# Performance work log

Hardware: AMD Instinct MI355X
Metric: run time of the kernel (lower is better)

## Reference

```python
import jax, jax.numpy as jnp
import numpy as np

LN_EPS = 1e-5

def _layernorm(x, gamma, beta):
    mu = jnp.mean(x, axis=-1, keepdims=True)
    var = jnp.mean((x - mu) ** 2, axis=-1, keepdims=True)
    return (x - mu) * jax.lax.rsqrt(var + LN_EPS) * gamma + beta

def setup_inputs() -> dict:
    key = jax.random.key(0)
    ks = jax.random.split(key, 12)
    n_drug, n_dis, E = 10000, 10000, 1000000
    feat = 128          # in_units * 2
    d_in = 2 * feat     # in_units * 4 = 256
    hid = 128
    hid2 = hid // 2
    def lin(kw, kb, fan_in, fan_out):
        bound = 1.0 / np.sqrt(fan_in)
        W = jax.random.uniform(kw, (fan_in, fan_out), jnp.float32, -bound, bound)
        b = jax.random.uniform(kb, (fan_out,), jnp.float32, -bound, bound)
        return W, b
    W1, b1 = lin(ks[0], ks[1], d_in, hid)
    W2, b2 = lin(ks[2], ks[3], hid, hid2)
    W3, b3 = lin(ks[4], ks[5], hid2, 1)
    return {
        "drug_feat": jax.random.normal(ks[6], (n_drug, feat), jnp.float32),
        "dis_feat": jax.random.normal(ks[7], (n_dis, feat), jnp.float32),
        "src_idx": jax.random.randint(ks[8], (E,), 0, n_drug, jnp.int32),
        "dst_idx": jax.random.randint(ks[9], (E,), 0, n_dis, jnp.int32),
        "W1": W1, "b1": b1,
        "g1": jnp.ones((hid,), jnp.float32), "be1": jnp.zeros((hid,), jnp.float32),
        "W2": W2, "b2": b2,
        "g2": jnp.ones((hid2,), jnp.float32), "be2": jnp.zeros((hid2,), jnp.float32),
        "W3": W3, "b3": b3,
    }

def reference(drug_feat, dis_feat, src_idx, dst_idx,
              W1, b1, g1, be1, W2, b2, g2, be2, W3, b3):
    # apply_edges: gather src (drug) and dst (disease) features, concat -> [E, 4*in_units]
    m = jnp.concatenate([drug_feat[src_idx], dis_feat[dst_idx]], axis=1)
    h = jax.nn.gelu(_layernorm(m @ W1 + b1, g1, be1), approximate=False)
    h = jax.nn.gelu(_layernorm(h @ W2 + b2, g2, be2), approximate=False)
    return h @ W3 + b3  # [E, 1]
```

## Files before the change

### kernel.cpp

```cpp
#include <hip/hip_runtime.h>
#include <hip/hip_bf16.h>

typedef __attribute__((ext_vector_type(4))) float f32x4;
typedef __attribute__((ext_vector_type(8))) short bf16x8;

#define MFMA16(a, b, c) __builtin_amdgcn_mfma_f32_16x16x32_bf16((a), (b), (c), 0, 0, 0)

#define W1T_OFF 0
#define B1_OFF  65536
#define G1_OFF  66048
#define E1_OFF  66560
#define B2_OFF  67072
#define G2_OFF  67328
#define E2_OFF  67584
#define W3_OFF  67840
#define B3_OFF  68096
#define SMEM_BYTES 68128

__device__ __forceinline__ short f2bf(float x) {
  __hip_bfloat16 h = __float2bfloat16(x);
  return __builtin_bit_cast(short, h);
}

__device__ __forceinline__ bf16x8 pack8(f32x4 a, f32x4 b) {
  bf16x8 r;
  r[0] = f2bf(a[0]); r[1] = f2bf(a[1]); r[2] = f2bf(a[2]); r[3] = f2bf(a[3]);
  r[4] = f2bf(b[0]); r[5] = f2bf(b[1]); r[6] = f2bf(b[2]); r[7] = f2bf(b[3]);
  return r;
}

__device__ __forceinline__ float gelu_fast(float z) {
  float s = z * z;
  float y = z * __builtin_fmaf(0.0705657f, s, 1.5976f);
  float t = __expf(-y);
  return z * __builtin_amdgcn_rcpf(1.0f + t);
}

__global__ __launch_bounds__(256) void prep_weights(
    const float* __restrict__ W1, const float* __restrict__ W2,
    short* __restrict__ w1i, short* __restrict__ w2i) {
  int idx = blockIdx.x * 256 + threadIdx.x;
  if (idx < 32768) {
    int k = idx >> 7, n = idx & 127;
    w1i[n * 256 + ((((k >> 3) ^ (n & 7)) << 3) | (k & 7))] = f2bf(W1[idx]);
  } else if (idx < 40960) {
    int j = idx - 32768;
    int n2 = j >> 7, pos = j & 127;
    int kf = ((((pos >> 3) ^ (n2 & 7)) << 3) | (pos & 7));
    int q = (kf >> 3) & 3, kb2 = kf >> 5, e = kf & 7;
    int n = kb2 * 32 + (e >> 2) * 16 + q * 4 + (e & 3);
    w2i[j] = f2bf(W2[n * 64 + n2]);
  }
}

__global__ __launch_bounds__(256) void prep_feats(
    const float* __restrict__ f, short* __restrict__ o, int n8) {
  int idx = blockIdx.x * 256 + threadIdx.x;
  if (idx < n8) {
    f32x4 a = *(const f32x4*)(f + idx * 8);
    f32x4 b = *(const f32x4*)(f + idx * 8 + 4);
    *(bf16x8*)(o + idx * 8) = pack8(a, b);
  }
}

__global__ __launch_bounds__(512, 2) void mlp_fused(
    const short* __restrict__ drugb, const short* __restrict__ disb,
    const int* __restrict__ src, const int* __restrict__ dst,
    const short* __restrict__ w1i, const short* __restrict__ w2i,
    const float* __restrict__ b1, const float* __restrict__ g1, const float* __restrict__ be1,
    const float* __restrict__ b2, const float* __restrict__ g2, const float* __restrict__ be2,
    const float* __restrict__ W3, const float* __restrict__ b3,
    float* __restrict__ out, int E, int ntiles) {
  extern __shared__ char smem[];
  short* w1t = (short*)(smem + W1T_OFF);
  float* b1s = (float*)(smem + B1_OFF);
  float* g1s = (float*)(smem + G1_OFF);
  float* e1s = (float*)(smem + E1_OFF);
  float* b2s = (float*)(smem + B2_OFF);
  float* g2s = (float*)(smem + G2_OFF);
  float* e2s = (float*)(smem + E2_OFF);
  float* w3s = (float*)(smem + W3_OFF);
  float* b3s = (float*)(smem + B3_OFF);

  const int tid  = threadIdx.x;
  const int wave = tid >> 6;
  const int lane = tid & 63;
  const int q    = lane >> 4;
  const int cc   = lane & 15;

  #pragma unroll
  for (int o = 0; o < 8; ++o) {
    int s = (tid + o * 512) * 8;
    *(bf16x8*)(w1t + s) = *(const bf16x8*)(w1i + s);
  }
  if (tid < 128) { b1s[tid] = b1[tid]; g1s[tid] = g1[tid]; e1s[tid] = be1[tid]; }
  else if (tid < 192) { int j = tid - 128; b2s[j] = b2[j]; g2s[j] = g2[j]; e2s[j] = be2[j]; w3s[j] = W3[j]; }
  if (tid == 256) b3s[0] = b3[0];
  __syncthreads();

  const short* w2p = w2i + cc * 128;

  for (int tile = blockIdx.x; tile < ntiles; tile += gridDim.x) {
    const int r  = tile * 128 + wave * 16 + cc;
    const int rc = (r < E) ? r : (E - 1);
    const short* pd = drugb + (size_t)src[rc] * 128 + q * 8;
    const short* pq = disb  + (size_t)dst[rc] * 128 + q * 8;

    f32x4 acc1[8];
    #pragma unroll
    for (int nt = 0; nt < 8; ++nt)
      acc1[nt] = *(const f32x4*)(b1s + nt * 16 + q * 4);

    bf16x8 u = *(const bf16x8*)pd;
    #pragma unroll 1
    for (int kb = 0; kb < 8; ++kb) {
      bf16x8 bfr = u;
      if (kb < 7) {
        const short* pn = (kb < 3) ? (pd + (kb + 1) * 32) : (pq + (kb - 3) * 32);
        u = *(const bf16x8*)pn;
      }
      const char* abase = (const char*)w1t + cc * 512 + ((((kb * 4 + q) ^ (cc & 7))) << 4);
      #pragma unroll
      for (int nt = 0; nt < 8; ++nt) {
        bf16x8 af = *(const bf16x8*)(abase + nt * 8192);
        acc1[nt] = MFMA16(af, bfr, acc1[nt]);
      }
    }

    bf16x8 hreg[4];
    {
      float s = 0.f, ss = 0.f;
      #pragma unroll
      for (int nt = 0; nt < 8; ++nt)
        #pragma unroll
        for (int j = 0; j < 4; ++j) { float v = acc1[nt][j]; s += v; ss += v * v; }
      s  += __shfl_xor(s, 16);  s  += __shfl_xor(s, 32);
      ss += __shfl_xor(ss, 16); ss += __shfl_xor(ss, 32);
      float mu   = s * 0.0078125f;
      float var  = ss * 0.0078125f - mu * mu;
      var = (var > 0.f) ? var : 0.f;
      float rstd = __builtin_amdgcn_rsqf(var + 1e-5f);

      #pragma unroll
      for (int h = 0; h < 4; ++h) {
        f32x4 glo = *(const f32x4*)(g1s + (2 * h) * 16 + q * 4);
        f32x4 elo = *(const f32x4*)(e1s + (2 * h) * 16 + q * 4);
        f32x4 ghi = *(const f32x4*)(g1s + (2 * h + 1) * 16 + q * 4);
        f32x4 ehi = *(const f32x4*)(e1s + (2 * h + 1) * 16 + q * 4);
        f32x4 a, b;
        #pragma unroll
        for (int j = 0; j < 4; ++j) {
          a[j] = gelu_fast(__builtin_fmaf((acc1[2 * h][j] - mu) * rstd, glo[j], elo[j]));
          b[j] = gelu_fast(__builtin_fmaf((acc1[2 * h + 1][j] - mu) * rstd, ghi[j], ehi[j]));
        }
        hreg[h] = pack8(a, b);
      }
    }

    f32x4 acc2[4];
    #pragma unroll
    for (int t = 0; t < 4; ++t)
      acc2[t] = *(const f32x4*)(b2s + t * 16 + q * 4);

    #pragma unroll
    for (int kb2 = 0; kb2 < 4; ++kb2) {
      bf16x8 hb = hreg[kb2];
      const int ch = ((kb2 * 4 + q) ^ (cc & 7));
      #pragma unroll
      for (int t = 0; t < 4; ++t) {
        bf16x8 af = *(const bf16x8*)(w2p + t * 2048 + ch * 8);
        acc2[t] = MFMA16(af, hb, acc2[t]);
      }
      __builtin_amdgcn_sched_barrier(0);
    }

    {
      float s = 0.f, ss = 0.f;
      #pragma unroll
      for (int t = 0; t < 4; ++t)
        #pragma unroll
        for (int j = 0; j < 4; ++j) { float v = acc2[t][j]; s += v; ss += v * v; }
      s  += __shfl_xor(s, 16);  s  += __shfl_xor(s, 32);
      ss += __shfl_xor(ss, 16); ss += __shfl_xor(ss, 32);
      float mu   = s * 0.015625f;
      float var  = ss * 0.015625f - mu * mu;
      var = (var > 0.f) ? var : 0.f;
      float rstd = __builtin_amdgcn_rsqf(var + 1e-5f);

      float dot = 0.f;
      #pragma unroll
      for (int t = 0; t < 4; ++t) {
        f32x4 gv = *(const f32x4*)(g2s + t * 16 + q * 4);
        f32x4 ev = *(const f32x4*)(e2s + t * 16 + q * 4);
        f32x4 wv = *(const f32x4*)(w3s + t * 16 + q * 4);
        #pragma unroll
        for (int j = 0; j < 4; ++j) {
          float zz = __builtin_fmaf((acc2[t][j] - mu) * rstd, gv[j], ev[j]);
          dot = __builtin_fmaf(gelu_fast(zz), wv[j], dot);
        }
      }
      dot += __shfl_xor(dot, 16); dot += __shfl_xor(dot, 32);
      if (q == 0 && r < E) out[r] = dot + b3s[0];
    }
  }
}

extern "C" void kernel_launch(void* const* d_in, const int* in_sizes, int n_in,
                              void* d_out, int out_size, void* d_ws, size_t ws_size,
                              hipStream_t stream) {
  const float* drug = (const float*)d_in[0];
  const float* dis  = (const float*)d_in[1];
  const int*   src  = (const int*)d_in[2];
  const int*   dst  = (const int*)d_in[3];
  const float* W1   = (const float*)d_in[4];
  const float* b1   = (const float*)d_in[5];
  const float* g1   = (const float*)d_in[6];
  const float* be1  = (const float*)d_in[7];
  const float* W2   = (const float*)d_in[8];
  const float* b2   = (const float*)d_in[9];
  const float* g2   = (const float*)d_in[10];
  const float* be2  = (const float*)d_in[11];
  const float* W3   = (const float*)d_in[12];
  const float* b3   = (const float*)d_in[13];
  float* out = (float*)d_out;

  const int E      = in_sizes[2];
  const int ndrug8 = in_sizes[0] / 8;
  const int ndis8  = in_sizes[1] / 8;
  const int ntiles = (E + 127) / 128;

  short* w1i   = (short*)d_ws;
  short* w2i   = w1i + 32768;
  short* drugb = w2i + 8192;
  short* disb  = drugb + (size_t)ndrug8 * 8;

  (void)hipFuncSetAttribute((const void*)mlp_fused,
                            hipFuncAttributeMaxDynamicSharedMemorySize, SMEM_BYTES);

  prep_weights<<<dim3(160), dim3(256), 0, stream>>>(W1, W2, w1i, w2i);
  prep_feats<<<dim3((ndrug8 + 255) / 256), dim3(256), 0, stream>>>(drug, drugb, ndrug8);
  prep_feats<<<dim3((ndis8 + 255) / 256), dim3(256), 0, stream>>>(dis, disb, ndis8);

  int grid = 512;
  if (ntiles < grid) grid = ntiles;
  mlp_fused<<<dim3(grid), dim3(512), SMEM_BYTES, stream>>>(
      drugb, disb, src, dst, w1i, w2i, b1, g1, be1, b2, g2, be2, W3, b3, out, E, ntiles);
}
```

Before: 251.0 us.

## Split W1 between LDS and lane-packed global loads, repack W2 for coalescing

Keeps only the first 192 K-rows of W1 in LDS and pre-packs the last 64 rows and all of W2 in lane-contiguous MFMA fragment order, so each lane reads them from global/L2 with a single coalesced 16-byte load. This shrinks LDS per block (about 68KB to 52KB) and removes the xor-swizzled W2 addressing. GELU now uses exp2 with prescaled constants. The cost is extra global traffic per tile for the W1 tail and W2 fragments, which relies on cache hits.

```diff
diff --git a/kernel.cpp b/kernel.cpp
--- a/kernel.cpp
+++ b/kernel.cpp
@@ -7,15 +7,15 @@
 #define MFMA16(a, b, c) __builtin_amdgcn_mfma_f32_16x16x32_bf16((a), (b), (c), 0, 0, 0)
 
 #define W1T_OFF 0
-#define B1_OFF  65536
-#define G1_OFF  66048
-#define E1_OFF  66560
-#define B2_OFF  67072
-#define G2_OFF  67328
-#define E2_OFF  67584
-#define W3_OFF  67840
-#define B3_OFF  68096
-#define SMEM_BYTES 68128
+#define B1_OFF  49152
+#define G1_OFF  49664
+#define E1_OFF  50176
+#define B2_OFF  50688
+#define G2_OFF  50944
+#define E2_OFF  51200
+#define W3_OFF  51456
+#define B3_OFF  51712
+#define SMEM_BYTES 51744
 
 __device__ __forceinline__ short f2bf(float x) {
   __hip_bfloat16 h = __float2bfloat16(x);
@@ -31,25 +31,37 @@
 
 __device__ __forceinline__ float gelu_fast(float z) {
   float s = z * z;
-  float y = z * __builtin_fmaf(0.0705657f, s, 1.5976f);
-  float t = __expf(-y);
+  float y = z * __builtin_fmaf(-0.10180479f, s, -2.3048496f);
+  float t = __builtin_amdgcn_exp2f(y);
   return z * __builtin_amdgcn_rcpf(1.0f + t);
 }
 
 __global__ __launch_bounds__(256) void prep_weights(
     const float* __restrict__ W1, const float* __restrict__ W2,
-    short* __restrict__ w1i, short* __restrict__ w2i) {
+    short* __restrict__ w1i, short* __restrict__ w1b, short* __restrict__ w2L) {
   int idx = blockIdx.x * 256 + threadIdx.x;
   if (idx < 32768) {
     int k = idx >> 7, n = idx & 127;
-    w1i[n * 256 + ((((k >> 3) ^ (n & 7)) << 3) | (k & 7))] = f2bf(W1[idx]);
+    int chunk = k >> 3, e = k & 7;
+    short v = f2bf(W1[idx]);
+    if (chunk < 24) {
+      int pos = (chunk & 24) | ((chunk & 7) ^ (n & 7));
+      w1i[n * 192 + pos * 8 + e] = v;
+    } else {
+      int kb = chunk >> 2;
+      int qq = chunk & 3;
+      int lane = qq * 16 + (n & 15);
+      int nt = n >> 4;
+      w1b[((kb - 6) * 8 + nt) * 512 + lane * 8 + e] = v;
+    }
   } else if (idx < 40960) {
     int j = idx - 32768;
-    int n2 = j >> 7, pos = j & 127;
-    int kf = ((((pos >> 3) ^ (n2 & 7)) << 3) | (pos & 7));
-    int q = (kf >> 3) & 3, kb2 = kf >> 5, e = kf & 7;
-    int n = kb2 * 32 + (e >> 2) * 16 + q * 4 + (e & 3);
-    w2i[j] = f2bf(W2[n * 64 + n2]);
+    int n = j >> 6, n2 = j & 63;
+    int kb2 = n >> 5;
+    int qf = (n >> 2) & 3;
+    int e = ((n >> 4) & 1) * 4 + (n & 3);
+    int t = n2 >> 4, cc2 = n2 & 15;
+    w2L[(kb2 * 4 + t) * 512 + (qf * 16 + cc2) * 8 + e] = f2bf(W2[j]);
   }
 }
 
@@ -66,7 +78,8 @@
 __global__ __launch_bounds__(512, 2) void mlp_fused(
     const short* __restrict__ drugb, const short* __restrict__ disb,
     const int* __restrict__ src, const int* __restrict__ dst,
-    const short* __restrict__ w1i, const short* __restrict__ w2i,
+    const short* __restrict__ w1i, const short* __restrict__ w1b,
+    const short* __restrict__ w2L,
     const float* __restrict__ b1, const float* __restrict__ g1, const float* __restrict__ be1,
     const float* __restrict__ b2, const float* __restrict__ g2, const float* __restrict__ be2,
     const float* __restrict__ W3, const float* __restrict__ b3,
@@ -89,7 +102,7 @@
   const int cc   = lane & 15;
 
   #pragma unroll
-  for (int o = 0; o < 8; ++o) {
+  for (int o = 0; o < 6; ++o) {
     int s = (tid + o * 512) * 8;
     *(bf16x8*)(w1t + s) = *(const bf16x8*)(w1i + s);
   }
@@ -98,7 +111,8 @@
   if (tid == 256) b3s[0] = b3[0];
   __syncthreads();
 
-  const short* w2p = w2i + cc * 128;
+  const short* w1bp = w1b + (lane << 3);
+  const short* w2p  = w2L + (lane << 3);
 
   for (int tile = blockIdx.x; tile < ntiles; tile += gridDim.x) {
     const int r  = tile * 128 + wave * 16 + cc;
@@ -113,18 +127,30 @@
 
     bf16x8 u = *(const bf16x8*)pd;
     #pragma unroll 1
-    for (int kb = 0; kb < 8; ++kb) {
+    for (int kb = 0; kb < 6; ++kb) {
       bf16x8 bfr = u;
-      if (kb < 7) {
+      {
         const short* pn = (kb < 3) ? (pd + (kb + 1) * 32) : (pq + (kb - 3) * 32);
         u = *(const bf16x8*)pn;
       }
-      const char* abase = (const char*)w1t + cc * 512 + ((((kb * 4 + q) ^ (cc & 7))) << 4);
+      const char* abase = (const char*)w1t + cc * 384 + ((((kb * 4 + q) ^ (cc & 7))) << 4);
       #pragma unroll
       for (int nt = 0; nt < 8; ++nt) {
-        bf16x8 af = *(const bf16x8*)(abase + nt * 8192);
+        bf16x8 af = *(const bf16x8*)(abase + nt * 6144);
         acc1[nt] = MFMA16(af, bfr, acc1[nt]);
       }
+    }
+    #pragma unroll
+    for (int kb = 6; kb < 8; ++kb) {
+      bf16x8 bfr = u;
+      if (kb < 7) u = *(const bf16x8*)(pq + 96);
+      const short* gb = w1bp + (kb - 6) * 4096;
+      #pragma unroll
+      for (int nt = 0; nt < 8; ++nt) {
+        bf16x8 af = *(const bf16x8*)(gb + nt * 512);
+        acc1[nt] = MFMA16(af, bfr, acc1[nt]);
+      }
+      __builtin_amdgcn_sched_barrier(0);
     }
 
     bf16x8 hreg[4];
@@ -165,10 +191,9 @@
     #pragma unroll
     for (int kb2 = 0; kb2 < 4; ++kb2) {
       bf16x8 hb = hreg[kb2];
-      const int ch = ((kb2 * 4 + q) ^ (cc & 7));
       #pragma unroll
       for (int t = 0; t < 4; ++t) {
-        bf16x8 af = *(const bf16x8*)(w2p + t * 2048 + ch * 8);
+        bf16x8 af = *(const bf16x8*)(w2p + (kb2 * 4 + t) * 512);
         acc2[t] = MFMA16(af, hb, acc2[t]);
       }
       __builtin_amdgcn_sched_barrier(0);
@@ -230,19 +255,18 @@
   const int ntiles = (E + 127) / 128;
 
   short* w1i   = (short*)d_ws;
-  short* w2i   = w1i + 32768;
-  short* drugb = w2i + 8192;
+  short* w1b   = w1i + 24576;
+  short* w2L   = w1b + 8192;
+  short* drugb = w2L + 8192;
   short* disb  = drugb + (size_t)ndrug8 * 8;
 
-  (void)hipFuncSetAttribute((const void*)mlp_fused,
-                            hipFuncAttributeMaxDynamicSharedMemorySize, SMEM_BYTES);
-
-  prep_weights<<<dim3(160), dim3(256), 0, stream>>>(W1, W2, w1i, w2i);
+  prep_weights<<<dim3(160), dim3(256), 0, stream>>>(W1, W2, w1i, w1b, w2L);
   prep_feats<<<dim3((ndrug8 + 255) / 256), dim3(256), 0, stream>>>(drug, drugb, ndrug8);
   prep_feats<<<dim3((ndis8 + 255) / 256), dim3(256), 0, stream>>>(dis, disb, ndis8);
 
   int grid = 512;
   if (ntiles < grid) grid = ntiles;
   mlp_fused<<<dim3(grid), dim3(512), SMEM_BYTES, stream>>>(
-      drugb, disb, src, dst, w1i, w2i, b1, g1, be1, b2, g2, be2, W3, b3, out, E, ntiles);
-}
+      drugb, disb, src, dst, w1i, w1b, w2L,
+      b1, g1, be1, b2, g2, be2, W3, b3, out, E, ntiles);
+}
```

Result: slower. 261.3 us (+4.1%).

## Use 1024-thread blocks with shared W1, coalesced W2 layout, exp2-based GELU

Applied to the files above, without the earlier changes.

Doubles the block size to 1024 threads (16 waves), so each block processes 256 edges per tile and one LDS copy of W1 serves twice as many waves. This halves per-block staging of W1 and doubles the number of edges per block sharing the same LDS budget. W2 is relaid out so each lane reads a contiguous 16-byte chunk (lane*8), making the global/L2 loads fully coalesced instead of swizzled strided reads. GELU folds the -log2(e) factor into its polynomial coefficients and calls exp2 directly, saving a multiply per element. The risk is fewer resident blocks per CU and tighter register limits under waves_per_eu(2).

```diff
diff --git a/kernel.cpp b/kernel.cpp
--- a/kernel.cpp
+++ b/kernel.cpp
@@ -31,25 +31,26 @@
 
 __device__ __forceinline__ float gelu_fast(float z) {
   float s = z * z;
-  float y = z * __builtin_fmaf(0.0705657f, s, 1.5976f);
-  float t = __expf(-y);
+  float y = z * __builtin_fmaf(-0.10180479f, s, -2.3048496f);
+  float t = __builtin_amdgcn_exp2f(y);
   return z * __builtin_amdgcn_rcpf(1.0f + t);
 }
 
 __global__ __launch_bounds__(256) void prep_weights(
     const float* __restrict__ W1, const float* __restrict__ W2,
-    short* __restrict__ w1i, short* __restrict__ w2i) {
+    short* __restrict__ w1i, short* __restrict__ w2L) {
   int idx = blockIdx.x * 256 + threadIdx.x;
   if (idx < 32768) {
     int k = idx >> 7, n = idx & 127;
     w1i[n * 256 + ((((k >> 3) ^ (n & 7)) << 3) | (k & 7))] = f2bf(W1[idx]);
   } else if (idx < 40960) {
     int j = idx - 32768;
-    int n2 = j >> 7, pos = j & 127;
-    int kf = ((((pos >> 3) ^ (n2 & 7)) << 3) | (pos & 7));
-    int q = (kf >> 3) & 3, kb2 = kf >> 5, e = kf & 7;
-    int n = kb2 * 32 + (e >> 2) * 16 + q * 4 + (e & 3);
-    w2i[j] = f2bf(W2[n * 64 + n2]);
+    int n = j >> 6, n2 = j & 63;
+    int kb2 = n >> 5;
+    int qf = (n >> 2) & 3;
+    int e = ((n >> 4) & 1) * 4 + (n & 3);
+    int t = n2 >> 4, cc2 = n2 & 15;
+    w2L[(kb2 * 4 + t) * 512 + (qf * 16 + cc2) * 8 + e] = f2bf(W2[j]);
   }
 }
 
@@ -63,10 +64,11 @@
   }
 }
 
-__global__ __launch_bounds__(512, 2) void mlp_fused(
+__global__ __launch_bounds__(1024) __attribute__((amdgpu_waves_per_eu(2)))
+void mlp_fused(
     const short* __restrict__ drugb, const short* __restrict__ disb,
     const int* __restrict__ src, const int* __restrict__ dst,
-    const short* __restrict__ w1i, const short* __restrict__ w2i,
+    const short* __restrict__ w1i, const short* __restrict__ w2L,
     const float* __restrict__ b1, const float* __restrict__ g1, const float* __restrict__ be1,
     const float* __restrict__ b2, const float* __restrict__ g2, const float* __restrict__ be2,
     const float* __restrict__ W3, const float* __restrict__ b3,
@@ -89,8 +91,8 @@
   const int cc   = lane & 15;
 
   #pragma unroll
-  for (int o = 0; o < 8; ++o) {
-    int s = (tid + o * 512) * 8;
+  for (int o = 0; o < 4; ++o) {
+    int s = (tid + o * 1024) * 8;
     *(bf16x8*)(w1t + s) = *(const bf16x8*)(w1i + s);
   }
   if (tid < 128) { b1s[tid] = b1[tid]; g1s[tid] = g1[tid]; e1s[tid] = be1[tid]; }
@@ -98,10 +100,10 @@
   if (tid == 256) b3s[0] = b3[0];
   __syncthreads();
 
-  const short* w2p = w2i + cc * 128;
+  const short* w2p = w2L + (lane << 3);
 
   for (int tile = blockIdx.x; tile < ntiles; tile += gridDim.x) {
-    const int r  = tile * 128 + wave * 16 + cc;
+    const int r  = tile * 256 + wave * 16 + cc;
     const int rc = (r < E) ? r : (E - 1);
     const short* pd = drugb + (size_t)src[rc] * 128 + q * 8;
     const short* pq = disb  + (size_t)dst[rc] * 128 + q * 8;
@@ -165,10 +167,9 @@
     #pragma unroll
     for (int kb2 = 0; kb2 < 4; ++kb2) {
       bf16x8 hb = hreg[kb2];
-      const int ch = ((kb2 * 4 + q) ^ (cc & 7));
       #pragma unroll
       for (int t = 0; t < 4; ++t) {
-        bf16x8 af = *(const bf16x8*)(w2p + t * 2048 + ch * 8);
+        bf16x8 af = *(const bf16x8*)(w2p + (kb2 * 4 + t) * 512);
         acc2[t] = MFMA16(af, hb, acc2[t]);
       }
       __builtin_amdgcn_sched_barrier(0);
@@ -227,22 +228,23 @@
   const int E      = in_sizes[2];
   const int ndrug8 = in_sizes[0] / 8;
   const int ndis8  = in_sizes[1] / 8;
-  const int ntiles = (E + 127) / 128;
+  const int ntiles = (E + 255) / 256;
 
   short* w1i   = (short*)d_ws;
-  short* w2i   = w1i + 32768;
-  short* drugb = w2i + 8192;
+  short* w2L   = w1i + 32768;
+  short* drugb = w2L + 8192;
   short* disb  = drugb + (size_t)ndrug8 * 8;
 
   (void)hipFuncSetAttribute((const void*)mlp_fused,
                             hipFuncAttributeMaxDynamicSharedMemorySize, SMEM_BYTES);
 
-  prep_weights<<<dim3(160), dim3(256), 0, stream>>>(W1, W2, w1i, w2i);
+  prep_weights<<<dim3(160), dim3(256), 0, stream>>>(W1, W2, w1i, w2L);
   prep_feats<<<dim3((ndrug8 + 255) / 256), dim3(256), 0, stream>>>(drug, drugb, ndrug8);
   prep_feats<<<dim3((ndis8 + 255) / 256), dim3(256), 0, stream>>>(dis, disb, ndis8);
 
   int grid = 512;
   if (ntiles < grid) grid = ntiles;
-  mlp_fused<<<dim3(grid), dim3(512), SMEM_BYTES, stream>>>(
-      drugb, disb, src, dst, w1i, w2i, b1, g1, be1, b2, g2, be2, W3, b3, out, E, ntiles);
-}
+  mlp_fused<<<dim3(grid), dim3(1024), SMEM_BYTES, stream>>>(
+      drugb, disb, src, dst, w1i, w2L,
+      b1, g1, be1, b2, g2, be2, W3, b3, out, E, ntiles);
+}
```

Result: no change. 247.5 us (-1.4%).
